# Optimization experiments

Hardware: AMD Instinct MI355X
Metric: run time of the kernel (lower is better)

## Reference

```python
import jax, jax.numpy as jnp
import numpy as np

N = 50000        # num nodes
E = 1600000      # num edges (avg degree 32)
DIN = 128        # dim_in
DOUT = 256       # dim_out
DA = 32          # dim_atten
SLOPE = 0.2      # leaky_relu negative slope


def setup_inputs() -> dict:
    key = jax.random.key(0)
    ks = jax.random.split(key, 9)
    x = jax.random.normal(ks[0], (N, DIN), dtype=jnp.float32)
    row = jax.random.randint(ks[1], (E,), 0, N, dtype=jnp.int32)
    col = jax.random.randint(ks[2], (E,), 0, N, dtype=jnp.int32)
    adj_val = jax.random.uniform(ks[3], (E,), dtype=jnp.float32)
    # learned params (Linear weights stored as [in, out] for x @ W)
    W_row = (jax.random.normal(ks[4], (DIN, DA)) / np.sqrt(DIN)).astype(jnp.float32)
    W_col = (jax.random.normal(ks[5], (DIN, DA)) / np.sqrt(DIN)).astype(jnp.float32)
    W_x = (jax.random.normal(ks[6], (DIN, DOUT)) / np.sqrt(DIN)).astype(jnp.float32)
    b_x = jnp.zeros((DOUT,), dtype=jnp.float32)
    return {"x": x, "row": row, "col": col, "adj_val": adj_val,
            "W_row": W_row, "W_col": W_col, "W_x": W_x, "b_x": b_x}


def reference(x, row, col, adj_val, W_row, W_col, W_x, b_x):
    # per-node attention projections
    a_row = x @ W_row                      # [N, DA]
    a_col = x @ W_col                      # [N, DA]
    # 'Multiply' attention: per-edge dot product scaled by rsqrt(DA)
    atten = jnp.sum(a_row[row] * a_col[col], axis=1) * jax.lax.rsqrt(jnp.float32(DA))  # [E]
    atten = jnp.where(atten >= 0, atten, SLOPE * atten)   # leaky_relu
    atten = jnp.exp(atten - jnp.max(atten))               # global-max-shifted exp
    # row-sum normalization (segment softmax denominator)
    deg = jax.ops.segment_sum(atten, row, num_segments=N)  # [N]
    atten = atten * (1.0 / (deg + 1e-15))[row]             # [E]
    # atten_combine == 'plus': average with original adjacency values
    vals = (adj_val + atten) * 0.5                         # [E]
    # sparse-dense matmul: out[i] = sum_{e: row[e]==i} vals[e] * x[col[e]]
    out = jax.ops.segment_sum(vals[:, None] * x[col], row, num_segments=N)  # [N, DIN]
    return out @ W_x + b_x                                 # [N, DOUT]
```

## Files before the change

kernel.cpp:

```cpp
#include <hip/hip_runtime.h>


#define DIN   128
#define DOUT  256
#define DA    32
#define SLOPE 0.2f
#define RSQRT_DA 0.17677669529663687f
#define BSH   6
#define BCAP  2560
#define CSTRIDE 32
#define NBMAX 800
#define PB_CHUNK 8192
#define NU    5

typedef unsigned int uint;
typedef unsigned short ushort;
typedef __attribute__((ext_vector_type(8))) short bf16x8;
typedef __attribute__((ext_vector_type(4))) float f32x4;

static __device__ __forceinline__ ushort f2bf(float f) {
  const uint u = __float_as_uint(f);
  return (ushort)((u + 0x7fffu + ((u >> 16) & 1u)) >> 16);
}

__global__ __launch_bounds__(256) void wconv_kernel(
    const float* __restrict__ Wx, ushort* __restrict__ wxt,
    const float* __restrict__ Wr, const float* __restrict__ Wc,
    ushort* __restrict__ wrct, int* __restrict__ bcursor, int nb) {
  __shared__ ushort s[16][DIN];
  const int t = threadIdx.x;
  const int b = blockIdx.x;
  if (b < 16) {
    const int c0 = b * 16;
#pragma unroll
    for (int u = 0; u < 8; ++u) {
      const int k = u * 16 + (t >> 4);
      s[t & 15][k] = f2bf(Wx[(size_t)k * DOUT + c0 + (t & 15)]);
    }
    __syncthreads();
    const int c = t >> 4;
    const int kk = (t & 15) * 8;
    *(uint4*)(wxt + (size_t)(c0 + c) * DIN + kk) = *(const uint4*)&s[c][kk];
  } else if (b < 20) {
    const int c = (b - 16) * 16 + (t >> 4);
    const int k0 = (t & 15) * 8;
    const float* src = (c < DA) ? (Wr + c) : (Wc + (c - DA));
    ushort h[8];
#pragma unroll
    for (int j = 0; j < 8; ++j) h[j] = f2bf(src[(size_t)(k0 + j) * DA]);
    uint4 v;
    v.x = (uint)h[0] | ((uint)h[1] << 16);
    v.y = (uint)h[2] | ((uint)h[3] << 16);
    v.z = (uint)h[4] | ((uint)h[5] << 16);
    v.w = (uint)h[6] | ((uint)h[7] << 16);
    *(uint4*)(wrct + (size_t)c * DIN + k0) = v;
  } else {
    for (int i = t; i < nb; i += 256) bcursor[i * CSTRIDE] = i * BCAP;
  }
}

__global__ __launch_bounds__(512) void super_kernel(
    const float* __restrict__ x, const ushort* __restrict__ wrct,
    float* __restrict__ a_row, ushort* __restrict__ a_colh,
    ushort* __restrict__ xh,
    const int* __restrict__ row, const int* __restrict__ col,
    const float* __restrict__ adj, int* __restrict__ bcursor,
    int2* __restrict__ ibuf, int nb, int E, int npart, int n) {
  __shared__ union {
    struct { int hist[NBMAX]; int base[NBMAX]; } p;
    ushort xb[32][136];
  } sh;
  const int t = threadIdx.x;

  if ((int)blockIdx.x < npart) {
    int* hist = sh.p.hist;
    int* base = sh.p.base;
    const int e0 = blockIdx.x * PB_CHUNK;
    for (int b = t; b < nb; b += 512) hist[b] = 0;
    __syncthreads();
    for (int u = 0; u < PB_CHUNK / 512; ++u) {
      const int e = e0 + u * 512 + t;
      if (e < E) atomicAdd(&hist[row[e] >> BSH], 1);
    }
    __syncthreads();
    for (int b = t; b < nb; b += 512) {
      const int c = hist[b];
      base[b] = c ? atomicAdd(&bcursor[b * CSTRIDE], c) : 0;
      hist[b] = 0;
    }
    __syncthreads();
    for (int u = 0; u < PB_CHUNK / 512; ++u) {
      const int e = e0 + u * 512 + t;
      if (e < E) {
        const int r = row[e];
        const int b = r >> BSH;
        const int pos = base[b] + atomicAdd(&hist[b], 1);
        ibuf[pos] = make_int2(((r & 63) << 16) | col[e], __float_as_int(adj[e]));
      }
    }
    return;
  }

  const int pb = blockIdx.x - npart;
  const int node0 = pb * 32;
  const float4* xg = (const float4*)(x + (size_t)node0 * DIN);
  if (node0 + 32 <= n) {
#pragma unroll
    for (int u = 0; u < 2; ++u) {
      const int f = t + u * 512;
      const float4 v = xg[f];
      ushort4 h;
      h.x = f2bf(v.x); h.y = f2bf(v.y); h.z = f2bf(v.z); h.w = f2bf(v.w);
      *(ushort4*)&sh.xb[f >> 5][(f & 31) * 4] = h;
      ((ushort4*)(xh + (size_t)node0 * DIN))[f] = h;
    }
  } else {
#pragma unroll
    for (int u = 0; u < 2; ++u) {
      const int f = t + u * 512;
      const int nd = node0 + (f >> 5);
      float4 v;
      if (nd < n) v = xg[f];
      else { v.x = 0.f; v.y = 0.f; v.z = 0.f; v.w = 0.f; }
      ushort4 h;
      h.x = f2bf(v.x); h.y = f2bf(v.y); h.z = f2bf(v.z); h.w = f2bf(v.w);
      *(ushort4*)&sh.xb[f >> 5][(f & 31) * 4] = h;
      if (nd < n) ((ushort4*)(xh + (size_t)node0 * DIN))[f] = h;
    }
  }
  __syncthreads();

  const int w = t >> 6;
  const int l = t & 63;
  const int lr = l & 15;
  const int lk = (l >> 4) * 8;
  const int h2 = w & 1;
  const int q = w >> 1;
  f32x4 acc = {0.f, 0.f, 0.f, 0.f};
#pragma unroll
  for (int kk = 0; kk < 4; ++kk) {
    const bf16x8 a = *(const bf16x8*)&sh.xb[h2 * 16 + lr][kk * 32 + lk];
    const bf16x8 bb =
        *(const bf16x8*)(wrct + (size_t)(q * 16 + lr) * DIN + kk * 32 + lk);
    acc = __builtin_amdgcn_mfma_f32_16x16x32_bf16(a, bb, acc, 0, 0, 0);
  }
  const int colq = q * 16 + lr;
  const int r0 = (l >> 4) * 4;
#pragma unroll
  for (int r = 0; r < 4; ++r) {
    const int node = node0 + h2 * 16 + r0 + r;
    if (node < n) {
      if (colq < DA)
        a_row[(size_t)node * DA + colq] = acc[r] * RSQRT_DA;
      else
        a_colh[(size_t)node * DA + (colq - DA)] = f2bf(acc[r]);
    }
  }
}

#define NODE_BODY(J)                                                    \
  {                                                                     \
    const int2 e = spk[w][half][(J)];                                   \
    const float pv = sp[w][half][(J)];                                  \
    const uint2 xv = xh2[(size_t)e.x * 32 + la];                        \
    const float av = __int_as_float(e.y);                               \
    const float f0 = __uint_as_float(xv.x << 16);                       \
    const float f1 = __uint_as_float(xv.x & 0xffff0000u);               \
    const float f2 = __uint_as_float(xv.y << 16);                       \
    const float f3 = __uint_as_float(xv.y & 0xffff0000u);               \
    aa0 += av * f0; aa1 += av * f1; aa2 += av * f2; aa3 += av * f3;     \
    ap0 += pv * f0; ap1 += pv * f1; ap2 += pv * f2; ap3 += pv * f3;     \
    deg += pv;                                                          \
  }

__global__ __launch_bounds__(512) void node_kernel(
    const uint* __restrict__ xh, const float* __restrict__ a_row,
    const ushort* __restrict__ a_colh, const int* __restrict__ bcursor,
    const int2* __restrict__ ibuf, ushort* __restrict__ feath, int n) {
  __shared__ int2  eL[BCAP];
  __shared__ int   cnt[64];
  __shared__ int   excl[65];
  __shared__ int2  spk[8][2][32];
  __shared__ float sp[8][2][32];
  __shared__ float s_ar[8][2][32];
  const int t = threadIdx.x;
  const int b = blockIdx.x;
  const int node0 = b << BSH;
  const int estart = b * BCAP;
  const int ecnt = bcursor[b * CSTRIDE] - estart;

  if (t < 64) cnt[t] = 0;
  __syncthreads();
  int2 myv[NU];
#pragma unroll
  for (int u = 0; u < NU; ++u) {
    const int e = u * 512 + t;
    if (e < ecnt) {
      myv[u] = ibuf[estart + e];
      atomicAdd(&cnt[myv[u].x >> 16], 1);
    }
  }
  __syncthreads();
  if (t < 64) {
    const int v = cnt[t];
    int inc = v;
#pragma unroll
    for (int ofs = 1; ofs < 64; ofs <<= 1) {
      const int o = __shfl_up(inc, ofs, 64);
      if (t >= ofs) inc += o;
    }
    excl[t] = inc - v;
    if (t == 63) excl[64] = inc;
    cnt[t] = 0;
  }
  __syncthreads();
#pragma unroll
  for (int u = 0; u < NU; ++u) {
    const int e = u * 512 + t;
    if (e < ecnt) {
      const int rl = myv[u].x >> 16;
      const int pos = excl[rl] + atomicAdd(&cnt[rl], 1);
      eL[pos] = make_int2(myv[u].x & 0xffff, myv[u].y);
    }
  }
  __syncthreads();

  const int w = t >> 6;
  const int lane = t & 63;
  const int half = lane >> 5;
  const int la = lane & 31;
  const uint2* xh2 = (const uint2*)xh;

  for (int pp = 0; pp < 4; ++pp) {
    const int rl0 = (pp * 8 + w) * 2;
    const int i = node0 + rl0 + half;
    const int o0 = excl[rl0];
    const int o1 = excl[rl0 + 1];
    const int o2 = excl[rl0 + 2];
    const int d0 = o1 - o0, d1 = o2 - o1;
    const int myoff = half ? o1 : o0;
    const int myd = half ? d1 : d0;
    const int dmax = max(d0, d1);
    s_ar[w][half][la] = (i < n) ? a_row[(size_t)i * DA + la] : 0.f;

    float aa0 = 0.f, aa1 = 0.f, aa2 = 0.f, aa3 = 0.f;
    float ap0 = 0.f, ap1 = 0.f, ap2 = 0.f, ap3 = 0.f;
    float deg = 0.f;

    for (int base = 0; base < dmax; base += 32) {
      const int m = myd - base;
      if (la < m) {
        const int2 e = eL[myoff + base + la];
        spk[w][half][la] = e;
        const uint4* ac = (const uint4*)(a_colh + (size_t)e.x * DA);
        const float* ar = s_ar[w][half];
        float dot = 0.f;
#pragma unroll
        for (int k = 0; k < 4; ++k) {
          const uint4 q = ac[k];
          const float* a = ar + k * 8;
          dot += __uint_as_float(q.x << 16) * a[0] +
                 __uint_as_float(q.x & 0xffff0000u) * a[1] +
                 __uint_as_float(q.y << 16) * a[2] +
                 __uint_as_float(q.y & 0xffff0000u) * a[3] +
                 __uint_as_float(q.z << 16) * a[4] +
                 __uint_as_float(q.z & 0xffff0000u) * a[5] +
                 __uint_as_float(q.w << 16) * a[6] +
                 __uint_as_float(q.w & 0xffff0000u) * a[7];
        }
        const float lg = (dot >= 0.f) ? dot : SLOPE * dot;
        sp[w][half][la] = __expf(lg);
      } else {
        spk[w][half][la] = make_int2(0, 0);
        sp[w][half][la] = 0.f;
      }
      const int mmax = min(32, dmax - base);
      int j = 0;
      for (; j + 8 <= mmax; j += 8) {
#pragma unroll
        for (int u = 0; u < 8; ++u) NODE_BODY(j + u)
      }
      for (; j < mmax; ++j) NODE_BODY(j)
    }
    if (i < n) {
      const float inv = 0.5f / (deg + 1e-15f);
      ushort4 h;
      h.x = f2bf(0.5f * aa0 + inv * ap0);
      h.y = f2bf(0.5f * aa1 + inv * ap1);
      h.z = f2bf(0.5f * aa2 + inv * ap2);
      h.w = f2bf(0.5f * aa3 + inv * ap3);
      *(ushort4*)(feath + (size_t)i * DIN + la * 4) = h;
    }
  }
}

__global__ __launch_bounds__(256) void gemm_kernel(
    const ushort* __restrict__ feath, const ushort* __restrict__ wxt,
    const float* __restrict__ bx, float* __restrict__ out) {
  const int t = threadIdx.x;
  const int w = t >> 6;
  const int l = t & 63;
  const int row0 = blockIdx.x * 16;
  const int lr = l & 15;
  const int lk = (l >> 4) * 8;
  const int col0 = w * 64;

  f32x4 acc[4] = {f32x4{0.f, 0.f, 0.f, 0.f}, f32x4{0.f, 0.f, 0.f, 0.f},
                  f32x4{0.f, 0.f, 0.f, 0.f}, f32x4{0.f, 0.f, 0.f, 0.f}};
  const ushort* Abase = feath + (size_t)(row0 + lr) * DIN + lk;
#pragma unroll
  for (int kk = 0; kk < 4; ++kk) {
    const bf16x8 a = *(const bf16x8*)(Abase + kk * 32);
#pragma unroll
    for (int ct = 0; ct < 4; ++ct) {
      const bf16x8 b =
          *(const bf16x8*)(wxt + (size_t)(col0 + ct * 16 + lr) * DIN + kk * 32 + lk);
      acc[ct] = __builtin_amdgcn_mfma_f32_16x16x32_bf16(a, b, acc[ct], 0, 0, 0);
    }
  }
  const int crow0 = row0 + (l >> 4) * 4;
#pragma unroll
  for (int ct = 0; ct < 4; ++ct) {
    const int c = col0 + ct * 16 + lr;
    const float bv = bx[c];
#pragma unroll
    for (int r = 0; r < 4; ++r)
      out[(size_t)(crow0 + r) * DOUT + c] = acc[ct][r] + bv;
  }
}

extern "C" void kernel_launch(void* const* d_in, const int* in_sizes, int n_in,
                              void* d_out, int out_size, void* d_ws, size_t ws_size,
                              hipStream_t stream) {
  const float* x   = (const float*)d_in[0];
  const int*   row = (const int*)d_in[1];
  const int*   col = (const int*)d_in[2];
  const float* adj = (const float*)d_in[3];
  const float* Wr  = (const float*)d_in[4];
  const float* Wc  = (const float*)d_in[5];
  const float* Wx  = (const float*)d_in[6];
  const float* bx  = (const float*)d_in[7];
  float* out = (float*)d_out;

  const int n = in_sizes[0] / DIN;
  const int E = in_sizes[1];
  const int nb = (n + 63) >> BSH;
  const int npart = (E + PB_CHUNK - 1) / PB_CHUNK;
  const int nproj = (n + 31) / 32;

  int* w4 = (int*)d_ws;
  float* a_row   = (float*)w4;  w4 += (size_t)n * DA;
  ushort* feath  = (ushort*)w4; w4 += (size_t)n * DIN / 2;
  ushort* a_colh = (ushort*)w4; w4 += (size_t)n * DA / 2;
  uint*   xh     = (uint*)w4;   w4 += (size_t)n * DIN / 2;
  int2*   ibuf   = (int2*)w4;   w4 += (size_t)nb * BCAP * 2;
  int*    bcursor= w4;          w4 += (size_t)nb * CSTRIDE;
  ushort* wxt    = (ushort*)w4; w4 += (size_t)DOUT * DIN / 2;
  ushort* wrct   = (ushort*)w4;

  wconv_kernel<<<21, 256, 0, stream>>>(Wx, wxt, Wr, Wc, wrct, bcursor, nb);
  super_kernel<<<npart + nproj, 512, 0, stream>>>(
      x, wrct, a_row, a_colh, (ushort*)xh, row, col, adj, bcursor, ibuf,
      nb, E, npart, n);
  node_kernel<<<nb, 512, 0, stream>>>(
      (const uint*)xh, a_row, a_colh, bcursor, ibuf, feath, n);
  gemm_kernel<<<n / 16, 256, 0, stream>>>(feath, wxt, bx, out);
}
```

Measured before the change: 255.3 us.

## Split partition and projection kernels; stage partitioned edges in LDS for coalesced writes

```diff
diff --git a/kernel.cpp b/kernel.cpp
--- a/kernel.cpp
+++ b/kernel.cpp
@@ -25,8 +25,7 @@
 
 __global__ __launch_bounds__(256) void wconv_kernel(
     const float* __restrict__ Wx, ushort* __restrict__ wxt,
-    const float* __restrict__ Wr, const float* __restrict__ Wc,
-    ushort* __restrict__ wrct, int* __restrict__ bcursor, int nb) {
+    int* __restrict__ bcursor, int nb) {
   __shared__ ushort s[16][DIN];
   const int t = threadIdx.x;
   const int b = blockIdx.x;
@@ -41,68 +40,90 @@
     const int c = t >> 4;
     const int kk = (t & 15) * 8;
     *(uint4*)(wxt + (size_t)(c0 + c) * DIN + kk) = *(const uint4*)&s[c][kk];
-  } else if (b < 20) {
-    const int c = (b - 16) * 16 + (t >> 4);
-    const int k0 = (t & 15) * 8;
-    const float* src = (c < DA) ? (Wr + c) : (Wc + (c - DA));
-    ushort h[8];
-#pragma unroll
-    for (int j = 0; j < 8; ++j) h[j] = f2bf(src[(size_t)(k0 + j) * DA]);
-    uint4 v;
-    v.x = (uint)h[0] | ((uint)h[1] << 16);
-    v.y = (uint)h[2] | ((uint)h[3] << 16);
-    v.z = (uint)h[4] | ((uint)h[5] << 16);
-    v.w = (uint)h[6] | ((uint)h[7] << 16);
-    *(uint4*)(wrct + (size_t)c * DIN + k0) = v;
   } else {
     for (int i = t; i < nb; i += 256) bcursor[i * CSTRIDE] = i * BCAP;
   }
 }
 
-__global__ __launch_bounds__(512) void super_kernel(
-    const float* __restrict__ x, const ushort* __restrict__ wrct,
-    float* __restrict__ a_row, ushort* __restrict__ a_colh,
-    ushort* __restrict__ xh,
+__global__ __launch_bounds__(512) void part_kernel(
     const int* __restrict__ row, const int* __restrict__ col,
     const float* __restrict__ adj, int* __restrict__ bcursor,
-    int2* __restrict__ ibuf, int nb, int E, int npart, int n) {
-  __shared__ union {
-    struct { int hist[NBMAX]; int base[NBMAX]; } p;
-    ushort xb[32][136];
-  } sh;
-  const int t = threadIdx.x;
-
-  if ((int)blockIdx.x < npart) {
-    int* hist = sh.p.hist;
-    int* base = sh.p.base;
-    const int e0 = blockIdx.x * PB_CHUNK;
-    for (int b = t; b < nb; b += 512) hist[b] = 0;
-    __syncthreads();
-    for (int u = 0; u < PB_CHUNK / 512; ++u) {
-      const int e = e0 + u * 512 + t;
-      if (e < E) atomicAdd(&hist[row[e] >> BSH], 1);
-    }
-    __syncthreads();
-    for (int b = t; b < nb; b += 512) {
-      const int c = hist[b];
-      base[b] = c ? atomicAdd(&bcursor[b * CSTRIDE], c) : 0;
-      hist[b] = 0;
-    }
-    __syncthreads();
-    for (int u = 0; u < PB_CHUNK / 512; ++u) {
-      const int e = e0 + u * 512 + t;
-      if (e < E) {
-        const int r = row[e];
-        const int b = r >> BSH;
-        const int pos = base[b] + atomicAdd(&hist[b], 1);
-        ibuf[pos] = make_int2(((r & 63) << 16) | col[e], __float_as_int(adj[e]));
+    int2* __restrict__ ibuf, int nb, int E) {
+  __shared__ int2 se[PB_CHUNK];
+  __shared__ int  hist[NBMAX];
+  __shared__ int  lscan[NBMAX];
+  __shared__ int  gbase[NBMAX];
+  const int t = threadIdx.x;
+  const int e0 = blockIdx.x * PB_CHUNK;
+  int myrow[PB_CHUNK / 512];
+  for (int b = t; b < nb; b += 512) hist[b] = 0;
+  __syncthreads();
+#pragma unroll
+  for (int u = 0; u < PB_CHUNK / 512; ++u) {
+    const int e = e0 + u * 512 + t;
+    myrow[u] = (e < E) ? row[e] : -1;
+    if (myrow[u] >= 0) atomicAdd(&hist[myrow[u] >> BSH], 1);
+  }
+  __syncthreads();
+  if (t < 64) {
+    int running = 0;
+    for (int base = 0; base < nb; base += 64) {
+      const int idx = base + t;
+      const int v = (idx < nb) ? hist[idx] : 0;
+      int inc = v;
+#pragma unroll
+      for (int ofs = 1; ofs < 64; ofs <<= 1) {
+        const int o = __shfl_up(inc, ofs, 64);
+        if (t >= ofs) inc += o;
       }
-    }
-    return;
-  }
-
-  const int pb = blockIdx.x - npart;
-  const int node0 = pb * 32;
+      if (idx < nb) lscan[idx] = running + inc - v;
+      running += __shfl(inc, 63, 64);
+    }
+  }
+  __syncthreads();
+  for (int b = t; b < nb; b += 512) {
+    const int c = hist[b];
+    gbase[b] = c ? atomicAdd(&bcursor[b * CSTRIDE], c) : 0;
+    hist[b] = 0;
+  }
+  __syncthreads();
+#pragma unroll
+  for (int u = 0; u < PB_CHUNK / 512; ++u) {
+    const int e = e0 + u * 512 + t;
+    if (myrow[u] >= 0) {
+      const int b = myrow[u] >> BSH;
+      const int pos = lscan[b] + atomicAdd(&hist[b], 1);
+      se[pos] = make_int2((b << 22) | ((myrow[u] & 63) << 16) | col[e],
+                          __float_as_int(adj[e]));
+    }
+  }
+  __syncthreads();
+  const int cnt_total = min(PB_CHUNK, E - e0);
+#pragma unroll
+  for (int u = 0; u < PB_CHUNK / 512; ++u) {
+    const int el = u * 512 + t;
+    if (el < cnt_total) {
+      const int2 v = se[el];
+      const int b = (int)((uint)v.x >> 22);
+      ibuf[gbase[b] + (el - lscan[b])] = make_int2(v.x & 0x3fffff, v.y);
+    }
+  }
+}
+
+__global__ __launch_bounds__(512) void proj_kernel(
+    const float* __restrict__ x, const float* __restrict__ Wr,
+    const float* __restrict__ Wc, float* __restrict__ a_row,
+    ushort* __restrict__ a_colh, ushort* __restrict__ xh, int n) {
+  __shared__ ushort xb[32][136];
+  __shared__ ushort wrc[64][136];
+  const int t = threadIdx.x;
+  for (int g = t; g < 64 * DIN; g += 512) {
+    const int c = g >> 7, k = g & 127;
+    const float v = (c < DA) ? Wr[(size_t)k * DA + c]
+                             : Wc[(size_t)k * DA + (c - DA)];
+    wrc[c][k] = f2bf(v);
+  }
+  const int node0 = blockIdx.x * 32;
   const float4* xg = (const float4*)(x + (size_t)node0 * DIN);
   if (node0 + 32 <= n) {
 #pragma unroll
@@ -111,7 +132,7 @@
       const float4 v = xg[f];
       ushort4 h;
       h.x = f2bf(v.x); h.y = f2bf(v.y); h.z = f2bf(v.z); h.w = f2bf(v.w);
-      *(ushort4*)&sh.xb[f >> 5][(f & 31) * 4] = h;
+      *(ushort4*)&xb[f >> 5][(f & 31) * 4] = h;
       ((ushort4*)(xh + (size_t)node0 * DIN))[f] = h;
     }
   } else {
@@ -124,7 +145,7 @@
       else { v.x = 0.f; v.y = 0.f; v.z = 0.f; v.w = 0.f; }
       ushort4 h;
       h.x = f2bf(v.x); h.y = f2bf(v.y); h.z = f2bf(v.z); h.w = f2bf(v.w);
-      *(ushort4*)&sh.xb[f >> 5][(f & 31) * 4] = h;
+      *(ushort4*)&xb[f >> 5][(f & 31) * 4] = h;
       if (nd < n) ((ushort4*)(xh + (size_t)node0 * DIN))[f] = h;
     }
   }
@@ -139,9 +160,8 @@
   f32x4 acc = {0.f, 0.f, 0.f, 0.f};
 #pragma unroll
   for (int kk = 0; kk < 4; ++kk) {
-    const bf16x8 a = *(const bf16x8*)&sh.xb[h2 * 16 + lr][kk * 32 + lk];
-    const bf16x8 bb =
-        *(const bf16x8*)(wrct + (size_t)(q * 16 + lr) * DIN + kk * 32 + lk);
+    const bf16x8 a = *(const bf16x8*)&xb[h2 * 16 + lr][kk * 32 + lk];
+    const bf16x8 bb = *(const bf16x8*)&wrc[q * 16 + lr][kk * 32 + lk];
     acc = __builtin_amdgcn_mfma_f32_16x16x32_bf16(a, bb, acc, 0, 0, 0);
   }
   const int colq = q * 16 + lr;
@@ -355,13 +375,12 @@
   uint*   xh     = (uint*)w4;   w4 += (size_t)n * DIN / 2;
   int2*   ibuf   = (int2*)w4;   w4 += (size_t)nb * BCAP * 2;
   int*    bcursor= w4;          w4 += (size_t)nb * CSTRIDE;
-  ushort* wxt    = (ushort*)w4; w4 += (size_t)DOUT * DIN / 2;
-  ushort* wrct   = (ushort*)w4;
-
-  wconv_kernel<<<21, 256, 0, stream>>>(Wx, wxt, Wr, Wc, wrct, bcursor, nb);
-  super_kernel<<<npart + nproj, 512, 0, stream>>>(
-      x, wrct, a_row, a_colh, (ushort*)xh, row, col, adj, bcursor, ibuf,
-      nb, E, npart, n);
+  ushort* wxt    = (ushort*)w4;
+
+  wconv_kernel<<<17, 256, 0, stream>>>(Wx, wxt, bcursor, nb);
+  part_kernel<<<npart, 512, 0, stream>>>(row, col, adj, bcursor, ibuf, nb, E);
+  proj_kernel<<<nproj, 512, 0, stream>>>(
+      x, Wr, Wc, a_row, a_colh, (ushort*)xh, n);
   node_kernel<<<nb, 512, 0, stream>>>(
       (const uint*)xh, a_row, a_colh, bcursor, ibuf, feath, n);
   gemm_kernel<<<n / 16, 256, 0, stream>>>(feath, wxt, bx, out);
```

New measurement: 270.1 us. 1.06x slower.

## Stage partition scatter in LDS and shrink edge records to 6 bytes

Applied to the files above, without the earlier changes.

```diff
diff --git a/kernel.cpp b/kernel.cpp
--- a/kernel.cpp
+++ b/kernel.cpp
@@ -65,37 +65,79 @@
     ushort* __restrict__ xh,
     const int* __restrict__ row, const int* __restrict__ col,
     const float* __restrict__ adj, int* __restrict__ bcursor,
-    int2* __restrict__ ibuf, int nb, int E, int npart, int n) {
+    uint* __restrict__ ibufk, ushort* __restrict__ ibufa,
+    int nb, int E, int npart, int n) {
   __shared__ union {
-    struct { int hist[NBMAX]; int base[NBMAX]; } p;
+    struct {
+      uint   sek[PB_CHUNK];
+      ushort sea[PB_CHUNK];
+      int hist[NBMAX];
+      int lscan[NBMAX];
+      int gbase[NBMAX];
+    } p;
     ushort xb[32][136];
   } sh;
   const int t = threadIdx.x;
 
   if ((int)blockIdx.x < npart) {
     int* hist = sh.p.hist;
-    int* base = sh.p.base;
+    int* lscan = sh.p.lscan;
+    int* gbase = sh.p.gbase;
     const int e0 = blockIdx.x * PB_CHUNK;
+    int myrow[PB_CHUNK / 512];
     for (int b = t; b < nb; b += 512) hist[b] = 0;
     __syncthreads();
+#pragma unroll
     for (int u = 0; u < PB_CHUNK / 512; ++u) {
       const int e = e0 + u * 512 + t;
-      if (e < E) atomicAdd(&hist[row[e] >> BSH], 1);
+      myrow[u] = (e < E) ? row[e] : -1;
+      if (myrow[u] >= 0) atomicAdd(&hist[myrow[u] >> BSH], 1);
+    }
+    __syncthreads();
+    if (t < 64) {
+      int running = 0;
+      for (int base = 0; base < nb; base += 64) {
+        const int idx = base + t;
+        const int v = (idx < nb) ? hist[idx] : 0;
+        int inc = v;
+#pragma unroll
+        for (int ofs = 1; ofs < 64; ofs <<= 1) {
+          const int o = __shfl_up(inc, ofs, 64);
+          if (t >= ofs) inc += o;
+        }
+        if (idx < nb) lscan[idx] = running + inc - v;
+        running += __shfl(inc, 63, 64);
+      }
     }
     __syncthreads();
     for (int b = t; b < nb; b += 512) {
       const int c = hist[b];
-      base[b] = c ? atomicAdd(&bcursor[b * CSTRIDE], c) : 0;
+      gbase[b] = c ? atomicAdd(&bcursor[b * CSTRIDE], c) : 0;
       hist[b] = 0;
     }
     __syncthreads();
+#pragma unroll
     for (int u = 0; u < PB_CHUNK / 512; ++u) {
       const int e = e0 + u * 512 + t;
-      if (e < E) {
-        const int r = row[e];
-        const int b = r >> BSH;
-        const int pos = base[b] + atomicAdd(&hist[b], 1);
-        ibuf[pos] = make_int2(((r & 63) << 16) | col[e], __float_as_int(adj[e]));
+      if (myrow[u] >= 0) {
+        const int b = myrow[u] >> BSH;
+        const int pos = lscan[b] + atomicAdd(&hist[b], 1);
+        sh.p.sek[pos] = ((uint)b << 22) | ((uint)(myrow[u] & 63) << 16) |
+                        (uint)col[e];
+        sh.p.sea[pos] = f2bf(adj[e]);
+      }
+    }
+    __syncthreads();
+    const int cnt_total = min(PB_CHUNK, E - e0);
+#pragma unroll
+    for (int u = 0; u < PB_CHUNK / 512; ++u) {
+      const int el = u * 512 + t;
+      if (el < cnt_total) {
+        const uint k = sh.p.sek[el];
+        const int b = (int)(k >> 22);
+        const int gpos = gbase[b] + (el - lscan[b]);
+        ibufk[gpos] = k & 0x3fffffu;
+        ibufa[gpos] = sh.p.sea[el];
       }
     }
     return;
@@ -160,10 +202,10 @@
 
 #define NODE_BODY(J)                                                    \
   {                                                                     \
-    const int2 e = spk[w][half][(J)];                                   \
+    const uint kv = spk[w][half][(J)];                                  \
     const float pv = sp[w][half][(J)];                                  \
-    const uint2 xv = xh2[(size_t)e.x * 32 + la];                        \
-    const float av = __int_as_float(e.y);                               \
+    const uint2 xv = xh2[(size_t)(kv & 0xffffu) * 32 + la];             \
+    const float av = __uint_as_float(kv & 0xffff0000u);                 \
     const float f0 = __uint_as_float(xv.x << 16);                       \
     const float f1 = __uint_as_float(xv.x & 0xffff0000u);               \
     const float f2 = __uint_as_float(xv.y << 16);                       \
@@ -176,13 +218,15 @@
 __global__ __launch_bounds__(512) void node_kernel(
     const uint* __restrict__ xh, const float* __restrict__ a_row,
     const ushort* __restrict__ a_colh, const int* __restrict__ bcursor,
-    const int2* __restrict__ ibuf, ushort* __restrict__ feath, int n) {
-  __shared__ int2  eL[BCAP];
-  __shared__ int   cnt[64];
-  __shared__ int   excl[65];
-  __shared__ int2  spk[8][2][32];
-  __shared__ float sp[8][2][32];
-  __shared__ float s_ar[8][2][32];
+    const uint* __restrict__ ibufk, const ushort* __restrict__ ibufa,
+    ushort* __restrict__ feath, int n) {
+  __shared__ uint   eLk[BCAP];
+  __shared__ ushort eLa[BCAP];
+  __shared__ int    cnt[64];
+  __shared__ int    excl[65];
+  __shared__ uint   spk[8][2][32];
+  __shared__ float  sp[8][2][32];
+  __shared__ float  s_ar[8][2][32];
   const int t = threadIdx.x;
   const int b = blockIdx.x;
   const int node0 = b << BSH;
@@ -191,13 +235,15 @@
 
   if (t < 64) cnt[t] = 0;
   __syncthreads();
-  int2 myv[NU];
+  uint   myk[NU];
+  ushort mya[NU];
 #pragma unroll
   for (int u = 0; u < NU; ++u) {
     const int e = u * 512 + t;
     if (e < ecnt) {
-      myv[u] = ibuf[estart + e];
-      atomicAdd(&cnt[myv[u].x >> 16], 1);
+      myk[u] = ibufk[estart + e];
+      mya[u] = ibufa[estart + e];
+      atomicAdd(&cnt[myk[u] >> 16], 1);
     }
   }
   __syncthreads();
@@ -218,9 +264,10 @@
   for (int u = 0; u < NU; ++u) {
     const int e = u * 512 + t;
     if (e < ecnt) {
-      const int rl = myv[u].x >> 16;
+      const int rl = (int)(myk[u] >> 16);
       const int pos = excl[rl] + atomicAdd(&cnt[rl], 1);
-      eL[pos] = make_int2(myv[u].x & 0xffff, myv[u].y);
+      eLk[pos] = myk[u] & 0xffffu;
+      eLa[pos] = mya[u];
     }
   }
   __syncthreads();
@@ -250,9 +297,10 @@
     for (int base = 0; base < dmax; base += 32) {
       const int m = myd - base;
       if (la < m) {
-        const int2 e = eL[myoff + base + la];
-        spk[w][half][la] = e;
-        const uint4* ac = (const uint4*)(a_colh + (size_t)e.x * DA);
+        const uint c = eLk[myoff + base + la];
+        const uint ah = (uint)eLa[myoff + base + la];
+        spk[w][half][la] = (ah << 16) | c;
+        const uint4* ac = (const uint4*)(a_colh + (size_t)c * DA);
         const float* ar = s_ar[w][half];
         float dot = 0.f;
 #pragma unroll
@@ -271,7 +319,7 @@
         const float lg = (dot >= 0.f) ? dot : SLOPE * dot;
         sp[w][half][la] = __expf(lg);
       } else {
-        spk[w][half][la] = make_int2(0, 0);
+        spk[w][half][la] = 0u;
         sp[w][half][la] = 0.f;
       }
       const int mmax = min(32, dmax - base);
@@ -353,16 +401,17 @@
   ushort* feath  = (ushort*)w4; w4 += (size_t)n * DIN / 2;
   ushort* a_colh = (ushort*)w4; w4 += (size_t)n * DA / 2;
   uint*   xh     = (uint*)w4;   w4 += (size_t)n * DIN / 2;
-  int2*   ibuf   = (int2*)w4;   w4 += (size_t)nb * BCAP * 2;
+  uint*   ibufk  = (uint*)w4;   w4 += (size_t)nb * BCAP;
+  ushort* ibufa  = (ushort*)w4; w4 += (size_t)nb * BCAP / 2;
   int*    bcursor= w4;          w4 += (size_t)nb * CSTRIDE;
   ushort* wxt    = (ushort*)w4; w4 += (size_t)DOUT * DIN / 2;
   ushort* wrct   = (ushort*)w4;
 
   wconv_kernel<<<21, 256, 0, stream>>>(Wx, wxt, Wr, Wc, wrct, bcursor, nb);
   super_kernel<<<npart + nproj, 512, 0, stream>>>(
-      x, wrct, a_row, a_colh, (ushort*)xh, row, col, adj, bcursor, ibuf,
-      nb, E, npart, n);
+      x, wrct, a_row, a_colh, (ushort*)xh, row, col, adj, bcursor,
+      ibufk, ibufa, nb, E, npart, n);
   node_kernel<<<nb, 512, 0, stream>>>(
-      (const uint*)xh, a_row, a_colh, bcursor, ibuf, feath, n);
+      (const uint*)xh, a_row, a_colh, bcursor, ibufk, ibufa, feath, n);
   gemm_kernel<<<n / 16, 256, 0, stream>>>(feath, wxt, bx, out);
 }
```

Result: faster. 249.3 us (-2.4%).
